# Kernel tuning notes

Measured on AMD Instinct MI355X. Metric: run time of the kernel, lower is better.

The kernel has to match this reference:

```python
import jax, jax.numpy as jnp
import numpy as np

BETA1, BETA2, BETA3 = 0.9, 0.8, 0.9
DECAY1, INC1 = 0.05, 5.0
DECAY3, INC3 = 0.05, 5.0
LATENCY = 4.0
B_CONST = 0.15
LIF1_MIN, LIF1_MAX = 150.0, 400.0
LIF3_MIN, LIF3_MAX = 50.0, 200.0
A_P, A_M, TAU_P, TAU_M = 0.01, 0.01, 20.0, 20.0  # exponential STDP params (params1/2/3)


def stdp(dt):
    # exponential STDP curve: potentiate when post fires after pre (dt>=0), depress otherwise
    return jnp.where(dt >= 0, A_P * jnp.exp(-dt / TAU_P), -A_M * jnp.exp(dt / TAU_M))


def setup_inputs() -> dict:
    key = jax.random.key(0)
    k1, k2, k3, k4 = jax.random.split(key, 4)
    H, N, C = 8192, 4096, 128
    return {
        "image": jax.random.uniform(k1, (N,), jnp.float32),
        "W1": jax.random.uniform(k2, (H, N), jnp.float32),
        "W2": jax.random.uniform(k3, (N, H), jnp.float32),
        "W3": jax.random.uniform(k4, (C, N), jnp.float32),
        "thr1": 100.0 * jnp.ones((H,), jnp.float32),
        "thr2": 5.0 * jnp.ones((N,), jnp.float32),
        "thr3": 100.0 * jnp.ones((C,), jnp.float32),
        "time": 256,
        "pw": 8,
    }


def reference(image, W1, W2, W3, thr1, thr2, thr3, time, pw):
    N = image.shape[0]
    H = W1.shape[0]
    C = W3.shape[0]
    T = int(time)
    Tf = jnp.float32(T)

    img_t = Tf * image  # input spike times, [N]
    # rate -> pulse encoding: input_spikes[t, i] = 1 for t in [floor(img_t[i]), floor(img_t[i])+pw)
    t_axis = jnp.arange(T, dtype=jnp.float32)[:, None]          # [T,1]
    start = jnp.floor(img_t)[None, :]                            # [1,N]
    input_spikes = ((t_axis >= start) & (t_axis < start + pw)).astype(jnp.float32)  # [T,N]

    def wta(mem, th):
        # winner-take-all (snntorch inhibition=True): only argmax neuron may spike
        j = jnp.argmax(mem)
        fire = (mem[j] > th[j]).astype(mem.dtype)
        return fire * jax.nn.one_hot(j, mem.shape[0], dtype=mem.dtype)

    def step(carry, xs):
        mem1, mem2, mem3, th1, th3, r1, r2, r3, hid_act, out_act = carry
        x, t = xs
        # layer 1: Leaky LIF, inhibition, reset-to-zero
        mem1 = BETA1 * mem1 + jnp.dot(W1, x)
        spk1 = wta(mem1, th1)
        mem1 = mem1 * (1.0 - spk1)
        # layer 2: Leaky LIF, no inhibition, reset-by-subtract
        mem2 = BETA2 * mem2 + jnp.dot(W2, spk1)
        spk2 = (mem2 > thr2).astype(mem2.dtype)
        mem2 = mem2 - spk2 * thr2
        # layer 3 (clustering): Leaky LIF, inhibition, zeroed after any spike
        mem3 = BETA3 * mem3 + jnp.dot(W3, spk2)
        spk3 = wta(mem3, th3)
        mem3 = mem3 - spk3 * th3
        mem3 = jnp.where(jnp.sum(spk3) > 0, 0.0, mem3)
        # first-spike-time recon (recon stays at first nonzero spk*(t+1))
        r1 = jnp.where(r1 != 0, r1, spk1 * (t + 1.0))
        r2 = jnp.where(r2 != 0, r2, spk2 * (t + 1.0))
        r3 = jnp.where(r3 != 0, r3, spk3 * (t + 1.0))
        hid_act = hid_act + spk1
        out_act = out_act + spk2
        # adaptive thresholds: homeostatic decay + spike-triggered increase, clamped
        th1 = jnp.clip(th1 - DECAY1 + INC1 * spk1, LIF1_MIN, LIF1_MAX)
        th3 = jnp.clip(th3 - DECAY3 + INC3 * spk3, LIF3_MIN, LIF3_MAX)
        return (mem1, mem2, mem3, th1, th3, r1, r2, r3, hid_act, out_act), None

    z = jnp.zeros
    carry0 = (z(H), z(N), z(C), thr1, thr3, z(H), z(N), z(C), z(H), z(N))
    (mem1, mem2, mem3, th1, th3, r1, r2, r3, hid_act, out_act), _ = jax.lax.scan(
        step, carry0, (input_spikes, jnp.arange(T, dtype=jnp.float32)))

    # neurons that never spiked get time T
    r1 = jnp.where(r1 == 0, Tf, r1)
    r2 = jnp.where(r2 == 0, Tf, r2)
    r3 = jnp.where(r3 == 0, Tf, r3)

    # STDP weight updates (exponential), same structure as PresentImage
    hid_mask = (hid_act > 0).astype(jnp.float32)
    delta_t1 = (r1[:, None] - img_t[None, :]) * hid_mask[:, None]      # [H,N]
    W1_new = W1 + stdp(delta_t1)
    delta_t2 = r2[:, None] - r1[None, :]                                # [N,H]
    zeta = (Tf - r1) * hid_mask / Tf                                    # [H]
    rho = (r2 - LATENCY - img_t) / Tf + B_CONST                         # [N]
    W2_new = jnp.clip(W2 + stdp(delta_t2) * (rho[:, None] * zeta[None, :]), 0.0, 1.0)
    delta_t3 = r3[:, None] - r2[None, :]                                # [C,N]
    W3_new = W3 + stdp(delta_t3)

    error = (img_t - (r2 - LATENCY)) / Tf
    error_scalar = jnp.sum(jnp.square(error))
    return (error, error_scalar, r1, r2, r3, W1_new, W2_new, W3_new)
```

## Files before the change

kernel.cpp:

```cpp
#include <hip/hip_runtime.h>
#include <cstdint>
#include <cstddef>

#define Hn 8192
#define Nn 4096
#define Cn 128
#define Tt 256
#define CAP 192

typedef unsigned long long ull;

__device__ __forceinline__ float th_lazy2(float b, float lo, float hi, int nup){
    if (nup <= 0) return b;
    float a = fminf(fmaxf(__fsub_rn(b, 0.05f), lo), hi);
    if (nup == 1) return a;
    return fmaxf(__fsub_rn(a, __fmul_rn(0.05f, (float)(nup - 1))), lo);
}

__device__ __forceinline__ float clamp01(float v){
    return fminf(fmaxf(v, 0.f), 1.f);
}

template<int CTRL>
__device__ __forceinline__ int dpp_i(int x, int old){
    return __builtin_amdgcn_update_dpp(old, x, CTRL, 0xf, 0xf, false);
}
__device__ __forceinline__ float wave_max_f(float v){
    const int NEG = __float_as_int(-3.4e38f);
#define STEPM(C) { float o = __int_as_float(dpp_i<C>(__float_as_int(v), NEG)); v = fmaxf(v, o); }
    STEPM(0x111) STEPM(0x112) STEPM(0x114) STEPM(0x118) STEPM(0x142) STEPM(0x143)
#undef STEPM
    return __int_as_float(__builtin_amdgcn_readlane(__float_as_int(v), 63));
}
__device__ __forceinline__ int wave_argmax_l(float bv, int bh, float &wv, int &wh){
    float v = wave_max_f(bv);
    ull tie = __ballot(bv == v);
    int tl = __ffsll((long long)tie) - 1;
    int h = __builtin_amdgcn_readlane(bh, tl);
    if (__builtin_expect(__popcll(tie) > 1, 0)){
        ull m = tie & (tie - 1);
        while (m){
            int l2 = __ffsll((long long)m) - 1;
            int h2 = __builtin_amdgcn_readlane(bh, l2);
            if (h2 < h){ h = h2; tl = l2; }
            m &= m - 1;
        }
    }
    wv = v; wh = h; return tl;
}
__device__ __forceinline__ float rl_f(float x, int l){
    return __int_as_float(__builtin_amdgcn_readlane(__float_as_int(x), l));
}

__global__ __launch_bounds__(1024) void k_prep(const float* __restrict__ image,
        int* __restrict__ boff, int* __restrict__ sidx, unsigned* __restrict__ anyv){
    __shared__ int s_start[Nn];
    __shared__ int s_c4[4][Tt];
    __shared__ int s_boff[Tt + 1];
    int tid = threadIdx.x;
    for (int i = tid; i < Nn; i += 1024)
        s_start[i] = (int)floorf(__fmul_rn(256.f, image[i]));
    if (tid < Tt) anyv[tid] = 0u;
    __syncthreads();
    int b = tid & 255, q = tid >> 8;
    {
        int c = 0;
        for (int k = 0; k < 1024; ++k) c += (s_start[q * 1024 + k] == b) ? 1 : 0;
        s_c4[q][b] = c;
    }
    __syncthreads();
    if (tid == 0){
        int acc = 0;
        for (int bb = 0; bb < Tt; ++bb){
            s_boff[bb] = acc;
            acc += s_c4[0][bb] + s_c4[1][bb] + s_c4[2][bb] + s_c4[3][bb];
        }
        s_boff[Tt] = acc;
    }
    __syncthreads();
    if (tid <= Tt) boff[tid] = s_boff[tid];
    int p = s_boff[b];
    if (q > 0) p += s_c4[0][b];
    if (q > 1) p += s_c4[1][b];
    if (q > 2) p += s_c4[2][b];
    for (int k = 0; k < 1024; ++k){
        int i = q * 1024 + k;
        if (s_start[i] == b) sidx[p++] = i;
    }
}

__global__ __launch_bounds__(256) void k_gbuckets(const float* __restrict__ W1,
        const int* __restrict__ boff, const int* __restrict__ sidx,
        float* __restrict__ G_T){
    __shared__ float rows[2][Nn];
    int tid = threadIdx.x;
    int h0 = blockIdx.x * 2;
    for (int r = 0; r < 2; ++r){
        const float4* src = (const float4*)(W1 + (size_t)(h0 + r) * Nn);
        float4* dst = (float4*)rows[r];
        for (int j = tid; j < Nn / 4; j += 256) dst[j] = src[j];
    }
    __syncthreads();
    int t = tid;
    int b0 = boff[t], b1 = boff[t + 1];
    float s0 = 0.f, s1 = 0.f;
    for (int k = b0; k < b1; ++k){
        int i = sidx[k];
        s0 += rows[0][i]; s1 += rows[1][i];
    }
    G_T[(size_t)(h0 + 0) * Tt + t] = s0;
    G_T[(size_t)(h0 + 1) * Tt + t] = s1;
}

__global__ __launch_bounds__(256) void k_c1M(const float* __restrict__ G_T,
        float* __restrict__ M, float* __restrict__ r1pre, float* __restrict__ o_r1){
    __shared__ float tile[32][Tt + 1];
    __shared__ float c1s[32][Tt + 1];
    const int tid = threadIdx.x;
    const int h0 = blockIdx.x * 32;
    for (int r = 0; r < 32; ++r) tile[r][tid] = G_T[(size_t)(h0 + r) * Tt + tid];
    __syncthreads();
    {
        int hs = tid & 31, ts = tid >> 5;
        for (int tb = 0; tb < 32; ++tb){
            int t = tb * 8 + ts;
            int lo = (t - 7 < 0) ? 0 : t - 7;
            float s = 0.f;
            for (int u = lo; u <= t; ++u) s += tile[hs][u];
            c1s[hs][t] = s;
        }
    }
    __syncthreads();
    if (tid < 32){
        float m = 0.f;
        for (int t = 0; t < Tt; ++t){
            m = __fadd_rn(__fmul_rn(0.9f, m), c1s[tid][t]);
            M[(size_t)t * Hn + h0 + tid] = m;
        }
        r1pre[h0 + tid] = 0.f;
        o_r1[h0 + tid] = 256.f;
    }
}

__global__ __launch_bounds__(256) void k_sel(const float* __restrict__ M,
        float4* __restrict__ cand){
    const int t = blockIdx.x, tid = threadIdx.x;
    __shared__ float s_row[Hn];
    __shared__ unsigned s_hist[256];
    __shared__ unsigned s_suf[256];
    __shared__ unsigned s_pref;
    __shared__ int s_rank;
    __shared__ int s_cnt;
    __shared__ int s_idx[CAP + 64];
    {
        const float4* src = (const float4*)(M + (size_t)t * Hn);
        float4* d4 = (float4*)s_row;
        for (int j = tid; j < Hn / 4; j += 256) d4[j] = src[j];
    }
    if (tid == 0){ s_pref = 0u; s_rank = CAP; s_cnt = 0; }
    __syncthreads();
#pragma unroll
    for (int b = 3; b >= 0; --b){
        s_hist[tid] = 0u;
        __syncthreads();
        unsigned pref = s_pref;
        int r = s_rank;
        for (int k = 0; k < 32; ++k){
            unsigned u = __float_as_uint(s_row[tid + (k << 8)]);
            bool match = (b == 3) ? true : ((u >> ((b + 1) * 8)) == pref);
            if (match) atomicAdd(&s_hist[(u >> (b * 8)) & 255], 1u);
        }
        __syncthreads();
        s_suf[tid] = s_hist[tid];
        __syncthreads();
#pragma unroll
        for (int off = 1; off < 256; off <<= 1){
            unsigned v = (tid + off < 256) ? s_suf[tid + off] : 0u;
            __syncthreads();
            s_suf[tid] += v;
            __syncthreads();
        }
        unsigned above = s_suf[tid] - s_hist[tid];
        if ((int)above < r && r <= (int)s_suf[tid]){
            s_pref = (pref << 8) | (unsigned)tid;
            s_rank = r - (int)above;
        }
        __syncthreads();
    }
    unsigned V = s_pref;
    for (int k = 0; k < 32; ++k){
        int i = tid + (k << 8);
        unsigned u = __float_as_uint(s_row[i]);
        if (u >= V){
            int p = atomicAdd(&s_cnt, 1);
            if (p < CAP + 64) s_idx[p] = i;
        }
    }
    __syncthreads();
    int c = s_cnt;
    bool ovf = (c > CAP);
    float vV = ovf ? 3.4e38f : __uint_as_float(V);
    for (int i = tid; i < CAP; i += 256){
        float4 e;
        if (!ovf && i < c){
            int ix = s_idx[i];
            e = make_float4(s_row[ix], __int_as_float(ix | (1 << 15)), 0.f, vV);
        } else {
            e = make_float4(-1.f, 0.f, 0.f, vV);
        }
        cand[(size_t)t * CAP + i] = e;
    }
}

__global__ __launch_bounds__(256) void k_w3t(const float* __restrict__ W3,
                                             float* __restrict__ W3T){
    __shared__ float tl[64][65];
    int bx = blockIdx.x & 63, by = blockIdx.x >> 6;
    int n0 = bx * 64, c0 = by * 64;
    int tid = threadIdx.x;
    for (int e = tid; e < 64 * 64; e += 256){
        int r = e >> 6, cc = e & 63;
        tl[r][cc] = W3[(size_t)(c0 + r) * Nn + n0 + cc];
    }
    __syncthreads();
    for (int e = tid; e < 64 * 64; e += 256){
        int rn = e >> 6, cc = e & 63;
        W3T[(size_t)(n0 + rn) * Cn + c0 + cc] = tl[cc][rn];
    }
}

#define NB_W1 1024
#define NB_W2 1024

__global__ __launch_bounds__(512, 4) void k_fused(
        const float* __restrict__ M, const float4* __restrict__ cand,
        const float* __restrict__ thr1,
        const float* __restrict__ W1, const float* __restrict__ W2,
        float* __restrict__ o_W1, float* __restrict__ o_W2,
        float* __restrict__ r1pre, float* __restrict__ o_r1,
        int* __restrict__ j1s){
    __shared__ float s_off[Hn];
    __shared__ float s_thb[Hn];
    __shared__ unsigned char s_ts[Hn];
    const int bid = blockIdx.x;
    const int tid = threadIdx.x;

    if (bid >= 1 && bid < 1 + NB_W1){
        size_t base = (size_t)(bid - 1) * 8192;
        const float4* src = (const float4*)W1;
        float4* dst = (float4*)o_W1;
        for (int i = tid; i < 8192; i += 512){
            float4 s = src[base + i];
            s.x = __fadd_rn(s.x, 0.01f); s.y = __fadd_rn(s.y, 0.01f);
            s.z = __fadd_rn(s.z, 0.01f); s.w = __fadd_rn(s.w, 0.01f);
            dst[base + i] = s;
        }
        return;
    }
    if (bid >= 1 + NB_W1){
        size_t base = (size_t)(bid - 1 - NB_W1) * 8192;
        const float4* src = (const float4*)W2;
        float4* dst = (float4*)o_W2;
        for (int i = tid; i < 8192; i += 512){
            float4 s = src[base + i];
            s.x = clamp01(s.x); s.y = clamp01(s.y);
            s.z = clamp01(s.z); s.w = clamp01(s.w);
            dst[base + i] = s;
        }
        return;
    }

    for (int h = tid; h < Hn; h += 512){
        s_off[h] = 0.f;
        s_thb[h] = thr1[h];
        s_ts[h] = 0;
    }
    __syncthreads();
    if (tid >= 64) return;
    const int lane = tid;
    const float Lc = -0.15200309344504997f;

    float4 cA0 = cand[lane],         cA1 = cand[64 + lane],         cA2 = cand[128 + lane];
    float4 cB0 = cand[CAP + lane],   cB1 = cand[CAP + 64 + lane],   cB2 = cand[CAP + 128 + lane];
    float4 cC0 = cand[2*CAP + lane], cC1 = cand[2*CAP + 64 + lane], cC2 = cand[2*CAP + 128 + lane];
    float4 gA0, gA1, gA2;
    {
        int h0 = __float_as_int(cA0.y) & 8191;
        int h1 = __float_as_int(cA1.y) & 8191;
        int h2 = __float_as_int(cA2.y) & 8191;
        gA0 = make_float4(s_off[h0], (float)s_ts[h0] - 1.f, s_thb[h0], 0.f);
        gA1 = make_float4(s_off[h1], (float)s_ts[h1] - 1.f, s_thb[h1], 0.f);
        gA2 = make_float4(s_off[h2], (float)s_ts[h2] - 1.f, s_thb[h2], 0.f);
    }

    for (int t = 0; t < Tt; ++t){
        const float tf = (float)t;
        float bm = -3.4e38f; int bhh = 0x7FFFFFFF;
        float braw = 0.f, bts = 0.f, bthb = 0.f;
#define CPROC(c) { \
        int mc = __float_as_int(cA##c.y); \
        int hc = mc & 8191; \
        float dd = __fsub_rn(tf, gA##c.y); \
        float mem = __fsub_rn(cA##c.x, __fmul_rn(exp2f(__fmul_rn(dd, Lc)), gA##c.x)); \
        if (!((mc >> 15) & 1)) mem = -3.4e38f; \
        if (mem > bm || (mem == bm && hc < bhh)){ bm = mem; bhh = hc; braw = cA##c.x; bts = gA##c.y; bthb = gA##c.z; } }
        CPROC(0) CPROC(1) CPROC(2)
#undef CPROC
        const int hB0 = __float_as_int(cB0.y) & 8191;
        const int hB1 = __float_as_int(cB1.y) & 8191;
        const int hB2 = __float_as_int(cB2.y) & 8191;
        float4 gB0 = make_float4(s_off[hB0], (float)s_ts[hB0] - 1.f, s_thb[hB0], 0.f);
        float4 gB1 = make_float4(s_off[hB1], (float)s_ts[hB1] - 1.f, s_thb[hB1], 0.f);
        float4 gB2 = make_float4(s_off[hB2], (float)s_ts[hB2] - 1.f, s_thb[hB2], 0.f);
        float wv; int wh;
        int wl = wave_argmax_l(bm, bhh, wv, wh);
        float raw = rl_f(braw, wl), tsv = rl_f(bts, wl), thb = rl_f(bthb, wl);
        const float vc = cA0.w;
        int skip = 0;
        if (wv < vc){
            if (t > 0 && vc < 150.f){
                skip = 1;
            } else {
                float fv = -3.4e38f; int fh = 0x7FFFFFFF;
                float fraw = 0.f, fts = 0.f, fthb = 0.f;
                const float4* Mrow4 = (const float4*)(M + (size_t)t * Hn);
                for (int q = 0; q < 32; ++q){
                    int e = q * 64 + lane;
                    float4 mv = Mrow4[e];
                    int ib = e * 4;
#define FPROC(comp, o2) { float x = mv.comp; int h2 = ib + o2; \
                    float gts = (float)s_ts[h2] - 1.f; \
                    float dd = __fsub_rn(tf, gts); \
                    float mm = __fsub_rn(x, __fmul_rn(exp2f(__fmul_rn(dd, Lc)), s_off[h2])); \
                    if (mm > fv || (mm == fv && h2 < fh)){ fv = mm; fh = h2; fraw = x; fts = gts; fthb = s_thb[h2]; } }
                    FPROC(x, 0) FPROC(y, 1) FPROC(z, 2) FPROC(w, 3)
#undef FPROC
                }
                wl = wave_argmax_l(fv, fh, wv, wh);
                raw = rl_f(fraw, wl); tsv = rl_f(fts, wl); thb = rl_f(fthb, wl);
            }
        }
        int fire = 0; float thnew = 0.f;
        if (!skip){
            float te = th_lazy2(thb, 150.f, 400.f, t - (int)tsv - 1);
            if (wv > te){
                fire = 1;
                thnew = fminf(fmaxf(__fadd_rn(__fsub_rn(te, 0.05f), 5.0f), 150.f), 400.f);
            }
        }
        if (fire){
            if (lane == 0){
                j1s[t] = wh;
                if (tsv < 0.f){ o_r1[wh] = tf + 1.f; r1pre[wh] = tf + 1.f; }
                s_off[wh] = raw;
                s_ts[wh] = (unsigned char)((t + 1 < 256) ? (t + 1) : 255);
                s_thb[wh] = thnew;
            }
            float4 upd = make_float4(raw, tf, thnew, 0.f);
            if (hB0 == wh) gB0 = upd;
            if (hB1 == wh) gB1 = upd;
            if (hB2 == wh) gB2 = upd;
        } else {
            if (lane == 0) j1s[t] = -1;
        }
        cA0 = cB0; cA1 = cB1; cA2 = cB2;
        cB0 = cC0; cB1 = cC1; cB2 = cC2;
        int tn = (t + 3 < Tt) ? t + 3 : Tt - 1;
        cC0 = cand[(size_t)tn * CAP + lane];
        cC1 = cand[(size_t)tn * CAP + 64 + lane];
        cC2 = cand[(size_t)tn * CAP + 128 + lane];
        gA0 = gB0; gA1 = gB1; gA2 = gB2;
    }
}

__global__ __launch_bounds__(256) void k_postmap(const int* __restrict__ j1s,
        int* __restrict__ j1slot, int* __restrict__ mh, int* __restrict__ nRout){
    __shared__ unsigned bm[256];
    __shared__ int s_j[Tt];
    __shared__ int pre[257];
    int tid = threadIdx.x;
    bm[tid] = 0u;
    s_j[tid] = j1s[tid];
    __syncthreads();
    int h = s_j[tid];
    if (h >= 0) atomicOr(&bm[h >> 5], 1u << (h & 31));
    __syncthreads();
    pre[tid + 1] = __popc(bm[tid]);
    if (tid == 0) pre[0] = 0;
    __syncthreads();
    for (int off = 1; off < 256; off <<= 1){
        int v = (tid + 1 > off) ? pre[tid + 1 - off] : 0;
        __syncthreads();
        pre[tid + 1] += v;
        __syncthreads();
    }
    {
        unsigned w = bm[tid]; int base = pre[tid];
        while (w){ int b = __ffs(w) - 1; w &= w - 1; mh[base++] = (tid << 5) | b; }
    }
    {
        int hh = s_j[tid];
        if (hh >= 0){
            int word = hh >> 5, bit = hh & 31;
            j1slot[tid] = pre[word] + __popc(bm[word] & ((1u << bit) - 1u));
        } else j1slot[tid] = -1;
    }
    if (tid == 0) *nRout = pre[256];
}

__global__ __launch_bounds__(256) void k_colg(const float* __restrict__ W2,
        const int* __restrict__ mh, const int* __restrict__ nRout,
        float* __restrict__ colv){
    int slot = blockIdx.x;
    if (slot >= *nRout) return;
    int h = mh[slot];
    int tid = threadIdx.x;
    float* dst = colv + (size_t)slot * Nn;
    for (int n = tid; n < Nn; n += 256) dst[n] = W2[(size_t)n * Hn + h];
}

__global__ __launch_bounds__(64) void k_lif2(const float* __restrict__ colv,
        const int* __restrict__ j1slot, const float* __restrict__ thr2,
        float* __restrict__ o_r2, ull* __restrict__ spkb, unsigned* __restrict__ anyv){
    __shared__ int s_j[Tt];
    int lane = threadIdx.x, blk = blockIdx.x;
    for (int i = lane; i < Tt; i += 64) s_j[i] = j1slot[i];
    __syncthreads();
    int n = blk * 64 + lane;
    float tv = thr2[n], m = 0.f, rp = 0.f;
    int s0v = s_j[0];
    float u0 = (s0v >= 0) ? colv[(size_t)s0v * Nn + n] : 0.f;
    for (int t = 0; t < Tt; ++t){
        float u1 = 0.f;
        if (t + 1 < Tt){
            int s1v = s_j[t + 1];
            if (s1v >= 0) u1 = colv[(size_t)s1v * Nn + n];
        }
        m = __fadd_rn(__fmul_rn(0.8f, m), u0);
        int f = 0;
        if (m > tv){
            m = __fsub_rn(m, tv);
            if (rp == 0.f) rp = (float)(t + 1);
            f = 1;
        }
        ull mask = __ballot(f);
        if (lane == 0){
            spkb[t * 64 + blk] = mask;
            if (mask) atomicOr(&anyv[t], 1u);
        }
        u0 = u1;
    }
    o_r2[n] = (rp == 0.f) ? 256.f : rp;
}

__global__ __launch_bounds__(128, 1) void k_sim3(const ull* __restrict__ spkb,
        const unsigned* __restrict__ anyv, const float* __restrict__ W3T,
        const float* __restrict__ thr3, float* __restrict__ o_r3){
    int tid = threadIdx.x, lane = tid & 63, w = tid >> 6;
    __shared__ unsigned s_any[Tt];
    __shared__ ull s_r2[2];
    __shared__ int s_fire;
    for (int i = tid; i < Tt; i += 128) s_any[i] = anyv[i];
    float m = 0.f, th0 = thr3[tid], rp = 0.f, thv = 0.f;
    int ts = -1, zero = 1;
    __syncthreads();
    for (int t = 0; t < Tt; ++t){
        if (zero && s_any[t] == 0u) continue;
        float d = 0.f;
        if (s_any[t]){
            for (int ww = 0; ww < 64; ++ww){
                ull bits = spkb[t * 64 + ww];
                while (bits){
                    int b2 = __ffsll((long long)bits) - 1;
                    bits &= bits - 1;
                    d = __fadd_rn(d, W3T[(size_t)(ww * 64 + b2) * Cn + tid]);
                }
            }
        }
        m = __fadd_rn(__fmul_rn(0.9f, m), d);
        ull k = (((ull)__float_as_uint(m >= 0.f ? m : 0.f)) << 32) | (unsigned)(8191 - tid);
        if (!(m >= 0.f)) k = (unsigned)(8191 - tid);
#pragma unroll
        for (int off = 32; off >= 1; off >>= 1){
            ull o = __shfl_down(k, off);
            if (o > k) k = o;
        }
        if (lane == 0) s_r2[w] = k;
        __syncthreads();
        ull wk = s_r2[0] > s_r2[1] ? s_r2[0] : s_r2[1];
        int wc = 8191 - (int)(wk & 0xFFFFu);
        float wv = __uint_as_float((unsigned)(wk >> 32));
        if (tid == wc){
            float te = (ts < 0) ? th_lazy2(th0, 50.f, 200.f, t)
                                : th_lazy2(thv, 50.f, 200.f, t - ts - 1);
            int f = (wv > te) ? 1 : 0;
            s_fire = f;
            if (f){
                thv = fminf(fmaxf(__fadd_rn(__fsub_rn(te, 0.05f), 5.0f), 50.f), 200.f);
                ts = t;
                if (rp == 0.f) rp = (float)(t + 1);
            }
        }
        __syncthreads();
        if (s_fire){ m = 0.f; zero = 1; }
        else zero = 0;
        __syncthreads();
    }
    o_r3[tid] = (rp == 0.f) ? 256.f : rp;
}

__global__ __launch_bounds__(1024) void k_scalars(const float* __restrict__ image,
        const float* __restrict__ r1pre, const float* __restrict__ o_r1,
        const float* __restrict__ o_r2,
        float* __restrict__ zeta, float* __restrict__ rho,
        float* __restrict__ imgt, float* __restrict__ eiP, float* __restrict__ eiM,
        float* __restrict__ Pv, float* __restrict__ Qv,
        float* __restrict__ E2P, float* __restrict__ E2M,
        float* __restrict__ o_err, float* __restrict__ o_es){
    int tid = threadIdx.x;
    for (int h = tid; h < Hn; h += 1024){
        float r1f = o_r1[h];
        float mask = (r1pre[h] != 0.f) ? 1.f : 0.f;
        float z = __fmul_rn(__fmul_rn(__fsub_rn(256.f, r1f), mask), 0.00390625f);
        zeta[h] = z;
        Pv[h] = __expf(r1f * 0.05f) * z;
        Qv[h] = __expf(-r1f * 0.05f) * z;
    }
    float acc = 0.f;
    for (int n = tid; n < Nn; n += 1024){
        float img = __fmul_rn(256.f, image[n]);
        float r2f = o_r2[n];
        float e = __fmul_rn(__fsub_rn(img, __fsub_rn(r2f, 4.0f)), 0.00390625f);
        o_err[n] = e;
        rho[n] = __fadd_rn(__fmul_rn(__fsub_rn(__fsub_rn(r2f, 4.0f), img), 0.00390625f), 0.15f);
        imgt[n] = img;
        eiP[n] = __expf(img * 0.05f);
        eiM[n] = __expf(-img * 0.05f);
        E2P[n] = __expf(r2f * 0.05f);
        E2M[n] = __expf(-r2f * 0.05f);
        acc = __fadd_rn(acc, __fmul_rn(e, e));
    }
    __shared__ float red[16];
    for (int off = 32; off >= 1; off >>= 1) acc += __shfl_down(acc, off);
    int lane = tid & 63, w = tid >> 6;
    if (lane == 0) red[w] = acc;
    __syncthreads();
    if (tid == 0){
        float s = 0.f;
        for (int q = 0; q < 16; ++q) s += red[q];
        *o_es = s;
    }
}

__global__ __launch_bounds__(256) void k_w1fix(const float* __restrict__ W1,
        const float* __restrict__ imgt, const float* __restrict__ eiP,
        const float* __restrict__ eiM, const float* __restrict__ o_r1,
        const int* __restrict__ mh, const int* __restrict__ nRout,
        float* __restrict__ o_W1){
    int slot = blockIdx.x;
    if (slot >= *nRout) return;
    int h = mh[slot];
    int tid = threadIdx.x;
    float r1f = o_r1[h];
    float a = 0.01f * __expf(-r1f * 0.05f);
    float b = 0.01f * __expf( r1f * 0.05f);
    const float4* src = (const float4*)(W1 + (size_t)h * Nn);
    float4* dst = (float4*)(o_W1 + (size_t)h * Nn);
    const float4* ig = (const float4*)imgt;
    const float4* p4 = (const float4*)eiP;
    const float4* m4 = (const float4*)eiM;
    for (int i = tid; i < Nn / 4; i += 256){
        float4 s = src[i];
        float4 im = ig[i], pp = p4[i], mm = m4[i];
        s.x += (r1f >= im.x) ? a * pp.x : -(b * mm.x);
        s.y += (r1f >= im.y) ? a * pp.y : -(b * mm.y);
        s.z += (r1f >= im.z) ? a * pp.z : -(b * mm.z);
        s.w += (r1f >= im.w) ? a * pp.w : -(b * mm.w);
        dst[i] = s;
    }
}

__global__ __launch_bounds__(128) void k_w2fix(
        const float* __restrict__ o_r1, const float* __restrict__ Pv,
        const float* __restrict__ Qv, const float* __restrict__ o_r2,
        const float* __restrict__ rho, const int* __restrict__ mh,
        const int* __restrict__ nRout, float* __restrict__ o_W2){
    __shared__ int   s_h[Tt];
    __shared__ float s_rv[Tt], s_pp[Tt], s_qq[Tt];
    int n = blockIdx.x, tid = threadIdx.x;
    int nRv = *nRout;
    for (int s = tid; s < nRv; s += 128){
        int h = mh[s];
        s_h[s] = h; s_rv[s] = o_r1[h]; s_pp[s] = Pv[h]; s_qq[s] = Qv[h];
    }
    __syncthreads();
    float r2f = o_r2[n], rh = rho[n];
    float A = 0.01f * rh * __expf(-r2f * 0.05f);
    float B = 0.01f * rh * __expf( r2f * 0.05f);
    for (int s = tid; s < nRv; s += 128){
        size_t idx = (size_t)n * Hn + s_h[s];
        float w = o_W2[idx];
        float rv = s_rv[s];
        w = clamp01(w + ((r2f >= rv) ? A * s_pp[s] : -(B * s_qq[s])));
        o_W2[idx] = w;
    }
}

__global__ __launch_bounds__(256) void k_w3new(const float* __restrict__ W3,
        const float* __restrict__ o_r2, const float* __restrict__ E2P,
        const float* __restrict__ E2M, const float* __restrict__ o_r3,
        float* __restrict__ o_W3){
    int c = blockIdx.x, tid = threadIdx.x;
    float r3f = o_r3[c];
    float a = 0.01f * __expf(-r3f * 0.05f);
    float b = 0.01f * __expf( r3f * 0.05f);
    const float4* src = (const float4*)(W3 + (size_t)c * Nn);
    float4* dst = (float4*)(o_W3 + (size_t)c * Nn);
    const float4* r24 = (const float4*)o_r2;
    const float4* p4 = (const float4*)E2P;
    const float4* m4 = (const float4*)E2M;
    for (int i = tid; i < Nn / 4; i += 256){
        float4 s = src[i]; float4 rv = r24[i]; float4 pp = p4[i]; float4 mm = m4[i];
        s.x += (r3f >= rv.x) ? a * pp.x : -(b * mm.x);
        s.y += (r3f >= rv.y) ? a * pp.y : -(b * mm.y);
        s.z += (r3f >= rv.z) ? a * pp.z : -(b * mm.z);
        s.w += (r3f >= rv.w) ? a * pp.w : -(b * mm.w);
        dst[i] = s;
    }
}

extern "C" void kernel_launch(void* const* d_in, const int* in_sizes, int n_in,
                              void* d_out, int out_size, void* d_ws, size_t ws_size,
                              hipStream_t stream){
    const float* image = (const float*)d_in[0];
    const float* W1   = (const float*)d_in[1];
    const float* W2   = (const float*)d_in[2];
    const float* W3   = (const float*)d_in[3];
    const float* thr1 = (const float*)d_in[4];
    const float* thr2 = (const float*)d_in[5];
    const float* thr3 = (const float*)d_in[6];

    float* out  = (float*)d_out;
    float* o_err = out;
    float* o_es  = out + 4096;
    float* o_r1  = out + 4097;
    float* o_r2  = out + 12289;
    float* o_r3  = out + 16385;
    float* o_W1  = out + 16513;
    float* o_W2  = o_W1 + (size_t)Hn * Nn;
    float* o_W3  = o_W2 + (size_t)Nn * Hn;

    float* ws = (float*)d_ws;
    float* G_T   = ws;
    float* M     = G_T + (size_t)Hn * Tt;
    float* W3T   = M + (size_t)Tt * Hn;
    float* colv  = W3T + (size_t)Nn * Cn;
    float4* cand = (float4*)(colv + (size_t)256 * Nn);
    ull* spkb    = (ull*)(cand + (size_t)Tt * CAP);
    float* r1pre = (float*)(spkb + (size_t)Tt * 64);
    float* zeta  = r1pre + Hn;
    float* rho   = zeta + Hn;
    float* imgt  = rho + Nn;
    float* eiP   = imgt + Nn;
    float* eiM   = eiP + Nn;
    float* Pv    = eiM + Nn;
    float* Qv    = Pv + Hn;
    float* E2P   = Qv + Hn;
    float* E2M   = E2P + Nn;
    int* boff   = (int*)(E2M + Nn);
    int* sidx   = boff + (Tt + 1);
    int* j1s    = sidx + Nn;
    int* j1slot = j1s + Tt;
    int* mh     = j1slot + Tt;
    int* nRout  = mh + 256;
    unsigned* anyv = (unsigned*)(nRout + 1);

    k_prep<<<1, 1024, 0, stream>>>(image, boff, sidx, anyv);
    k_gbuckets<<<Hn / 2, 256, 0, stream>>>(W1, boff, sidx, G_T);
    k_c1M<<<Hn / 32, 256, 0, stream>>>(G_T, M, r1pre, o_r1);
    k_sel<<<Tt, 256, 0, stream>>>(M, cand);
    k_w3t<<<128, 256, 0, stream>>>(W3, W3T);
    k_fused<<<1 + NB_W1 + NB_W2, 512, 0, stream>>>(
        M, cand, thr1, W1, W2, o_W1, o_W2, r1pre, o_r1, j1s);
    k_postmap<<<1, 256, 0, stream>>>(j1s, j1slot, mh, nRout);
    k_colg<<<256, 256, 0, stream>>>(W2, mh, nRout, colv);
    k_lif2<<<Nn / 64, 64, 0, stream>>>(colv, j1slot, thr2, o_r2, spkb, anyv);
    k_sim3<<<1, 128, 0, stream>>>(spkb, anyv, W3T, thr3, o_r3);
    k_scalars<<<1, 1024, 0, stream>>>(image, r1pre, o_r1, o_r2, zeta, rho,
                                      imgt, eiP, eiM, Pv, Qv, E2P, E2M, o_err, o_es);
    k_w1fix<<<256, 256, 0, stream>>>(W1, imgt, eiP, eiM, o_r1, mh, nRout, o_W1);
    k_w2fix<<<Nn, 128, 0, stream>>>(o_r1, Pv, Qv, o_r2, rho, mh, nRout, o_W2);
    k_w3new<<<Cn, 256, 0, stream>>>(W3, o_r2, E2P, E2M, o_r3, o_W3);
}
```

Before: 563.5 us.

## Fold W3 transpose and spike postmap into fused kernel, drop column gather

Moves the W3 transpose into extra blocks of the fused kernel, sharing its shared memory through a union. The hidden-spike bitmap and prefix sum that built mh/nRout now run at the tail of the serial block using wave shuffles. The separate postmap and column-gather kernels are removed. k_lif2 now reads W2 rows directly using the raw spike indices, with a 4-step software prefetch. This cuts three launches and an intermediate buffer, at the cost of strided per-thread row reads in lif2 and a larger shared-memory footprint, with launch bounds loosened to (512,1), for all fused blocks.

```diff
diff --git a/kernel.cpp b/kernel.cpp
--- a/kernel.cpp
+++ b/kernel.cpp
@@ -212,36 +212,30 @@
     }
 }
 
-__global__ __launch_bounds__(256) void k_w3t(const float* __restrict__ W3,
-                                             float* __restrict__ W3T){
-    __shared__ float tl[64][65];
-    int bx = blockIdx.x & 63, by = blockIdx.x >> 6;
-    int n0 = bx * 64, c0 = by * 64;
-    int tid = threadIdx.x;
-    for (int e = tid; e < 64 * 64; e += 256){
-        int r = e >> 6, cc = e & 63;
-        tl[r][cc] = W3[(size_t)(c0 + r) * Nn + n0 + cc];
-    }
-    __syncthreads();
-    for (int e = tid; e < 64 * 64; e += 256){
-        int rn = e >> 6, cc = e & 63;
-        W3T[(size_t)(n0 + rn) * Cn + c0 + cc] = tl[cc][rn];
-    }
-}
-
 #define NB_W1 1024
 #define NB_W2 1024
-
-__global__ __launch_bounds__(512, 4) void k_fused(
+#define NB_W3T 128
+
+union FusedLDS {
+    struct {
+        float off[Hn];
+        float thb[Hn];
+        unsigned char ts[Hn];
+        int j1[Tt];
+        unsigned bm[256];
+    } w;
+    float tl[64][65];
+};
+
+__global__ __launch_bounds__(512, 1) void k_fused(
         const float* __restrict__ M, const float4* __restrict__ cand,
         const float* __restrict__ thr1,
         const float* __restrict__ W1, const float* __restrict__ W2,
-        float* __restrict__ o_W1, float* __restrict__ o_W2,
+        const float* __restrict__ W3,
+        float* __restrict__ o_W1, float* __restrict__ o_W2, float* __restrict__ W3T,
         float* __restrict__ r1pre, float* __restrict__ o_r1,
-        int* __restrict__ j1s){
-    __shared__ float s_off[Hn];
-    __shared__ float s_thb[Hn];
-    __shared__ unsigned char s_ts[Hn];
+        int* __restrict__ j1s, int* __restrict__ mh, int* __restrict__ nRout){
+    __shared__ FusedLDS u;
     const int bid = blockIdx.x;
     const int tid = threadIdx.x;
 
@@ -257,7 +251,7 @@
         }
         return;
     }
-    if (bid >= 1 + NB_W1){
+    if (bid >= 1 + NB_W1 && bid < 1 + NB_W1 + NB_W2){
         size_t base = (size_t)(bid - 1 - NB_W1) * 8192;
         const float4* src = (const float4*)W2;
         float4* dst = (float4*)o_W2;
@@ -269,11 +263,26 @@
         }
         return;
     }
+    if (bid >= 1 + NB_W1 + NB_W2){
+        int r = bid - 1 - NB_W1 - NB_W2;
+        int bx = r & 63, by = r >> 6;
+        int n0 = bx * 64, c0 = by * 64;
+        for (int e = tid; e < 64 * 64; e += 512){
+            int rr = e >> 6, cc = e & 63;
+            u.tl[rr][cc] = W3[(size_t)(c0 + rr) * Nn + n0 + cc];
+        }
+        __syncthreads();
+        for (int e = tid; e < 64 * 64; e += 512){
+            int rn = e >> 6, cc = e & 63;
+            W3T[(size_t)(n0 + rn) * Cn + c0 + cc] = u.tl[cc][rn];
+        }
+        return;
+    }
 
     for (int h = tid; h < Hn; h += 512){
-        s_off[h] = 0.f;
-        s_thb[h] = thr1[h];
-        s_ts[h] = 0;
+        u.w.off[h] = 0.f;
+        u.w.thb[h] = thr1[h];
+        u.w.ts[h] = 0;
     }
     __syncthreads();
     if (tid >= 64) return;
@@ -283,15 +292,11 @@
     float4 cA0 = cand[lane],         cA1 = cand[64 + lane],         cA2 = cand[128 + lane];
     float4 cB0 = cand[CAP + lane],   cB1 = cand[CAP + 64 + lane],   cB2 = cand[CAP + 128 + lane];
     float4 cC0 = cand[2*CAP + lane], cC1 = cand[2*CAP + 64 + lane], cC2 = cand[2*CAP + 128 + lane];
-    float4 gA0, gA1, gA2;
-    {
-        int h0 = __float_as_int(cA0.y) & 8191;
-        int h1 = __float_as_int(cA1.y) & 8191;
-        int h2 = __float_as_int(cA2.y) & 8191;
-        gA0 = make_float4(s_off[h0], (float)s_ts[h0] - 1.f, s_thb[h0], 0.f);
-        gA1 = make_float4(s_off[h1], (float)s_ts[h1] - 1.f, s_thb[h1], 0.f);
-        gA2 = make_float4(s_off[h2], (float)s_ts[h2] - 1.f, s_thb[h2], 0.f);
-    }
+    float gofA0, gofA1, gofA2, gtsA0, gtsA1, gtsA2, gthA0, gthA1, gthA2;
+#define GATHA(c) { int hh = __float_as_int(cA##c.y) & 8191; \
+        gofA##c = u.w.off[hh]; gtsA##c = (float)u.w.ts[hh] - 1.f; gthA##c = u.w.thb[hh]; }
+    GATHA(0) GATHA(1) GATHA(2)
+#undef GATHA
 
     for (int t = 0; t < Tt; ++t){
         const float tf = (float)t;
@@ -300,24 +305,24 @@
 #define CPROC(c) { \
         int mc = __float_as_int(cA##c.y); \
         int hc = mc & 8191; \
-        float dd = __fsub_rn(tf, gA##c.y); \
-        float mem = __fsub_rn(cA##c.x, __fmul_rn(exp2f(__fmul_rn(dd, Lc)), gA##c.x)); \
+        float dd = __fsub_rn(tf, gtsA##c); \
+        float mem = __fsub_rn(cA##c.x, __fmul_rn(exp2f(__fmul_rn(dd, Lc)), gofA##c)); \
         if (!((mc >> 15) & 1)) mem = -3.4e38f; \
-        if (mem > bm || (mem == bm && hc < bhh)){ bm = mem; bhh = hc; braw = cA##c.x; bts = gA##c.y; bthb = gA##c.z; } }
+        if (mem > bm || (mem == bm && hc < bhh)){ bm = mem; bhh = hc; braw = cA##c.x; bts = gtsA##c; bthb = gthA##c; } }
         CPROC(0) CPROC(1) CPROC(2)
 #undef CPROC
-        const int hB0 = __float_as_int(cB0.y) & 8191;
-        const int hB1 = __float_as_int(cB1.y) & 8191;
-        const int hB2 = __float_as_int(cB2.y) & 8191;
-        float4 gB0 = make_float4(s_off[hB0], (float)s_ts[hB0] - 1.f, s_thb[hB0], 0.f);
-        float4 gB1 = make_float4(s_off[hB1], (float)s_ts[hB1] - 1.f, s_thb[hB1], 0.f);
-        float4 gB2 = make_float4(s_off[hB2], (float)s_ts[hB2] - 1.f, s_thb[hB2], 0.f);
+        int hB0 = __float_as_int(cB0.y) & 8191;
+        int hB1 = __float_as_int(cB1.y) & 8191;
+        int hB2 = __float_as_int(cB2.y) & 8191;
+        float gofB0 = u.w.off[hB0], gtsB0 = (float)u.w.ts[hB0] - 1.f, gthB0 = u.w.thb[hB0];
+        float gofB1 = u.w.off[hB1], gtsB1 = (float)u.w.ts[hB1] - 1.f, gthB1 = u.w.thb[hB1];
+        float gofB2 = u.w.off[hB2], gtsB2 = (float)u.w.ts[hB2] - 1.f, gthB2 = u.w.thb[hB2];
         float wv; int wh;
         int wl = wave_argmax_l(bm, bhh, wv, wh);
         float raw = rl_f(braw, wl), tsv = rl_f(bts, wl), thb = rl_f(bthb, wl);
         const float vc = cA0.w;
         int skip = 0;
-        if (wv < vc){
+        if (__builtin_expect(wv < vc, 0)){
             if (t > 0 && vc < 150.f){
                 skip = 1;
             } else {
@@ -329,15 +334,15 @@
                     float4 mv = Mrow4[e];
                     int ib = e * 4;
 #define FPROC(comp, o2) { float x = mv.comp; int h2 = ib + o2; \
-                    float gts = (float)s_ts[h2] - 1.f; \
+                    float gts = (float)u.w.ts[h2] - 1.f; \
                     float dd = __fsub_rn(tf, gts); \
-                    float mm = __fsub_rn(x, __fmul_rn(exp2f(__fmul_rn(dd, Lc)), s_off[h2])); \
-                    if (mm > fv || (mm == fv && h2 < fh)){ fv = mm; fh = h2; fraw = x; fts = gts; fthb = s_thb[h2]; } }
+                    float mm = __fsub_rn(x, __fmul_rn(exp2f(__fmul_rn(dd, Lc)), u.w.off[h2])); \
+                    if (mm > fv || (mm == fv && h2 < fh)){ fv = mm; fh = h2; fraw = x; fts = gts; fthb = u.w.thb[h2]; } }
                     FPROC(x, 0) FPROC(y, 1) FPROC(z, 2) FPROC(w, 3)
 #undef FPROC
                 }
                 wl = wave_argmax_l(fv, fh, wv, wh);
-                raw = rl_f(fraw, wl); tsv = rl_f(fts, wl); thb = rl_f(fthb, wl);
+                raw = rl_f(fraw, wl); tsv = rl_f(fts, wl); fthb = rl_f(fthb, wl); thb = fthb;
             }
         }
         int fire = 0; float thnew = 0.f;
@@ -350,18 +355,18 @@
         }
         if (fire){
             if (lane == 0){
+                u.w.j1[t] = wh;
                 j1s[t] = wh;
                 if (tsv < 0.f){ o_r1[wh] = tf + 1.f; r1pre[wh] = tf + 1.f; }
-                s_off[wh] = raw;
-                s_ts[wh] = (unsigned char)((t + 1 < 256) ? (t + 1) : 255);
-                s_thb[wh] = thnew;
+                u.w.off[wh] = raw;
+                u.w.ts[wh] = (unsigned char)((t + 1 < 256) ? (t + 1) : 255);
+                u.w.thb[wh] = thnew;
             }
-            float4 upd = make_float4(raw, tf, thnew, 0.f);
-            if (hB0 == wh) gB0 = upd;
-            if (hB1 == wh) gB1 = upd;
-            if (hB2 == wh) gB2 = upd;
+            if (hB0 == wh){ gofB0 = raw; gtsB0 = tf; gthB0 = thnew; }
+            if (hB1 == wh){ gofB1 = raw; gtsB1 = tf; gthB1 = thnew; }
+            if (hB2 == wh){ gofB2 = raw; gtsB2 = tf; gthB2 = thnew; }
         } else {
-            if (lane == 0) j1s[t] = -1;
+            if (lane == 0){ u.w.j1[t] = -1; j1s[t] = -1; }
         }
         cA0 = cB0; cA1 = cB1; cA2 = cB2;
         cB0 = cC0; cB1 = cC1; cB2 = cC2;
@@ -369,87 +374,64 @@
         cC0 = cand[(size_t)tn * CAP + lane];
         cC1 = cand[(size_t)tn * CAP + 64 + lane];
         cC2 = cand[(size_t)tn * CAP + 128 + lane];
-        gA0 = gB0; gA1 = gB1; gA2 = gB2;
-    }
-}
-
-__global__ __launch_bounds__(256) void k_postmap(const int* __restrict__ j1s,
-        int* __restrict__ j1slot, int* __restrict__ mh, int* __restrict__ nRout){
-    __shared__ unsigned bm[256];
-    __shared__ int s_j[Tt];
-    __shared__ int pre[257];
-    int tid = threadIdx.x;
-    bm[tid] = 0u;
-    s_j[tid] = j1s[tid];
-    __syncthreads();
-    int h = s_j[tid];
-    if (h >= 0) atomicOr(&bm[h >> 5], 1u << (h & 31));
-    __syncthreads();
-    pre[tid + 1] = __popc(bm[tid]);
-    if (tid == 0) pre[0] = 0;
-    __syncthreads();
-    for (int off = 1; off < 256; off <<= 1){
-        int v = (tid + 1 > off) ? pre[tid + 1 - off] : 0;
-        __syncthreads();
-        pre[tid + 1] += v;
-        __syncthreads();
-    }
-    {
-        unsigned w = bm[tid]; int base = pre[tid];
-        while (w){ int b = __ffs(w) - 1; w &= w - 1; mh[base++] = (tid << 5) | b; }
-    }
-    {
-        int hh = s_j[tid];
-        if (hh >= 0){
-            int word = hh >> 5, bit = hh & 31;
-            j1slot[tid] = pre[word] + __popc(bm[word] & ((1u << bit) - 1u));
-        } else j1slot[tid] = -1;
-    }
-    if (tid == 0) *nRout = pre[256];
-}
-
-__global__ __launch_bounds__(256) void k_colg(const float* __restrict__ W2,
-        const int* __restrict__ mh, const int* __restrict__ nRout,
-        float* __restrict__ colv){
-    int slot = blockIdx.x;
-    if (slot >= *nRout) return;
-    int h = mh[slot];
-    int tid = threadIdx.x;
-    float* dst = colv + (size_t)slot * Nn;
-    for (int n = tid; n < Nn; n += 256) dst[n] = W2[(size_t)n * Hn + h];
-}
-
-__global__ __launch_bounds__(64) void k_lif2(const float* __restrict__ colv,
-        const int* __restrict__ j1slot, const float* __restrict__ thr2,
+        gofA0 = gofB0; gtsA0 = gtsB0; gthA0 = gthB0;
+        gofA1 = gofB1; gtsA1 = gtsB1; gthA1 = gthB1;
+        gofA2 = gofB2; gtsA2 = gtsB2; gthA2 = gthB2;
+    }
+
+    for (int i = lane; i < 256; i += 64) u.w.bm[i] = 0u;
+    asm volatile("s_waitcnt lgkmcnt(0)" ::: "memory");
+    for (int i = lane; i < Tt; i += 64){
+        int h = u.w.j1[i];
+        if (h >= 0) atomicOr(&u.w.bm[h >> 5], 1u << (h & 31));
+    }
+    asm volatile("s_waitcnt lgkmcnt(0)" ::: "memory");
+    unsigned w0 = u.w.bm[lane*4+0], w1 = u.w.bm[lane*4+1];
+    unsigned w2 = u.w.bm[lane*4+2], w3 = u.w.bm[lane*4+3];
+    int c = __popc(w0) + __popc(w1) + __popc(w2) + __popc(w3);
+    int inc = c;
+#pragma unroll
+    for (int off = 1; off < 64; off <<= 1){
+        int v = __shfl_up(inc, off);
+        if (lane >= off) inc += v;
+    }
+    int b = inc - c;
+#define WALK(wrd, k) { unsigned ww = wrd; while (ww){ int bt = __ffs(ww) - 1; ww &= ww - 1; \
+        mh[b++] = ((lane * 4 + k) << 5) | bt; } }
+    WALK(w0, 0) WALK(w1, 1) WALK(w2, 2) WALK(w3, 3)
+#undef WALK
+    if (lane == 63) *nRout = inc;
+}
+
+__global__ __launch_bounds__(64) void k_lif2(const float* __restrict__ W2,
+        const int* __restrict__ j1s, const float* __restrict__ thr2,
         float* __restrict__ o_r2, ull* __restrict__ spkb, unsigned* __restrict__ anyv){
     __shared__ int s_j[Tt];
     int lane = threadIdx.x, blk = blockIdx.x;
-    for (int i = lane; i < Tt; i += 64) s_j[i] = j1slot[i];
+    for (int i = lane; i < Tt; i += 64) s_j[i] = j1s[i];
     __syncthreads();
     int n = blk * 64 + lane;
+    const float* Wrow = W2 + (size_t)n * Hn;
     float tv = thr2[n], m = 0.f, rp = 0.f;
-    int s0v = s_j[0];
-    float u0 = (s0v >= 0) ? colv[(size_t)s0v * Nn + n] : 0.f;
-    for (int t = 0; t < Tt; ++t){
-        float u1 = 0.f;
-        if (t + 1 < Tt){
-            int s1v = s_j[t + 1];
-            if (s1v >= 0) u1 = colv[(size_t)s1v * Nn + n];
-        }
-        m = __fadd_rn(__fmul_rn(0.8f, m), u0);
-        int f = 0;
-        if (m > tv){
-            m = __fsub_rn(m, tv);
-            if (rp == 0.f) rp = (float)(t + 1);
-            f = 1;
-        }
-        ull mask = __ballot(f);
-        if (lane == 0){
-            spkb[t * 64 + blk] = mask;
-            if (mask) atomicOr(&anyv[t], 1u);
-        }
-        u0 = u1;
-    }
+#define LD(dst, tt) { int hh = s_j[tt]; dst = (hh >= 0) ? Wrow[hh] : 0.f; }
+#define STEP(uu, tt) { m = __fadd_rn(__fmul_rn(0.8f, m), uu); int f = 0; \
+        if (m > tv){ m = __fsub_rn(m, tv); if (rp == 0.f) rp = (float)((tt) + 1); f = 1; } \
+        ull mask = __ballot(f); \
+        if (lane == 0){ spkb[(tt) * 64 + blk] = mask; if (mask) atomicOr(&anyv[tt], 1u); } }
+    float u0, u1, u2, u3;
+    LD(u0, 0) LD(u1, 1) LD(u2, 2) LD(u3, 3)
+    for (int g = 0; g < 64; ++g){
+        float v0 = 0.f, v1 = 0.f, v2 = 0.f, v3 = 0.f;
+        if (g < 63){
+            int bb = (g + 1) * 4;
+            LD(v0, bb) LD(v1, bb + 1) LD(v2, bb + 2) LD(v3, bb + 3)
+        }
+        int t = g * 4;
+        STEP(u0, t) STEP(u1, t + 1) STEP(u2, t + 2) STEP(u3, t + 3)
+        u0 = v0; u1 = v1; u2 = v2; u3 = v3;
+    }
+#undef LD
+#undef STEP
     o_r2[n] = (rp == 0.f) ? 256.f : rp;
 }
 
@@ -654,8 +636,7 @@
     float* G_T   = ws;
     float* M     = G_T + (size_t)Hn * Tt;
     float* W3T   = M + (size_t)Tt * Hn;
-    float* colv  = W3T + (size_t)Nn * Cn;
-    float4* cand = (float4*)(colv + (size_t)256 * Nn);
+    float4* cand = (float4*)(W3T + (size_t)Nn * Cn);
     ull* spkb    = (ull*)(cand + (size_t)Tt * CAP);
     float* r1pre = (float*)(spkb + (size_t)Tt * 64);
     float* zeta  = r1pre + Hn;
@@ -670,8 +651,7 @@
     int* boff   = (int*)(E2M + Nn);
     int* sidx   = boff + (Tt + 1);
     int* j1s    = sidx + Nn;
-    int* j1slot = j1s + Tt;
-    int* mh     = j1slot + Tt;
+    int* mh     = j1s + Tt;
     int* nRout  = mh + 256;
     unsigned* anyv = (unsigned*)(nRout + 1);
 
@@ -679,12 +659,9 @@
     k_gbuckets<<<Hn / 2, 256, 0, stream>>>(W1, boff, sidx, G_T);
     k_c1M<<<Hn / 32, 256, 0, stream>>>(G_T, M, r1pre, o_r1);
     k_sel<<<Tt, 256, 0, stream>>>(M, cand);
-    k_w3t<<<128, 256, 0, stream>>>(W3, W3T);
-    k_fused<<<1 + NB_W1 + NB_W2, 512, 0, stream>>>(
-        M, cand, thr1, W1, W2, o_W1, o_W2, r1pre, o_r1, j1s);
-    k_postmap<<<1, 256, 0, stream>>>(j1s, j1slot, mh, nRout);
-    k_colg<<<256, 256, 0, stream>>>(W2, mh, nRout, colv);
-    k_lif2<<<Nn / 64, 64, 0, stream>>>(colv, j1slot, thr2, o_r2, spkb, anyv);
+    k_fused<<<1 + NB_W1 + NB_W2 + NB_W3T, 512, 0, stream>>>(
+        M, cand, thr1, W1, W2, W3, o_W1, o_W2, W3T, r1pre, o_r1, j1s, mh, nRout);
+    k_lif2<<<Nn / 64, 64, 0, stream>>>(W2, j1s, thr2, o_r2, spkb, anyv);
     k_sim3<<<1, 128, 0, stream>>>(spkb, anyv, W3T, thr3, o_r3);
     k_scalars<<<1, 1024, 0, stream>>>(image, r1pre, o_r1, o_r2, zeta, rho,
                                       imgt, eiP, eiM, Pv, Qv, E2P, E2M, o_err, o_es);
```

After: 542.1 us. 3.8% less time.
